# Kernel tuning notes

Measured on AMD Instinct MI355X. Metric: run time of the kernel, lower is better.

## Reference

```python
import jax, jax.numpy as jnp
import numpy as np

B, P, H, W, D, C = 16, 4, 32, 32, 32, 8


def setup_inputs() -> dict:
    key = jax.random.key(0)
    k1, k2 = jax.random.split(key)
    input_fmap = jax.random.normal(k1, (B, P, H, W, D, C), dtype=jnp.float32)
    # identity affine + small noise so sampled coords mostly stay in-volume
    ident = jnp.concatenate([jnp.eye(3, dtype=jnp.float32), jnp.zeros((3, 1), jnp.float32)], axis=1)
    theta = ident[None, None] + 0.05 * jax.random.normal(k2, (B, P, 3, 4), dtype=jnp.float32)
    return {"input_fmap": input_fmap, "theta": theta}


def _affine_grid(theta, H, W, D):
    # matches tf.meshgrid default 'xy' indexing: shapes (H, W, D)
    x = jnp.arange(W, dtype=jnp.float32)
    y = jnp.arange(H, dtype=jnp.float32)
    z = jnp.arange(D, dtype=jnp.float32)
    xt, yt, zt = jnp.meshgrid(x, y, z, indexing='xy')  # each (H, W, D)
    grid = jnp.stack([xt.ravel(), yt.ravel(), zt.ravel(), jnp.ones(H * W * D, jnp.float32)], axis=0)  # (4, HWD)
    bg = jnp.einsum('bpij,jn->bpin', theta, grid)  # (B, P, 3, HWD)
    return bg.reshape(theta.shape[0], theta.shape[1], 3, H, W, D)


def reference(input_fmap, theta):
    Bb, Pp, Hh, Ww, Dd, Cc = input_fmap.shape
    bg = _affine_grid(theta, Hh, Ww, Dd)
    x = bg[:, :, 0] + 2.0  # (B, P, H, W, D)
    y = bg[:, :, 1] + 2.0
    z = bg[:, :, 2] + 2.0
    padded = jnp.pad(input_fmap, ((0, 0), (0, 0), (2, 2), (2, 2), (2, 2), (0, 0)))
    # faithful to original: all three axes clipped with H+2 (cubic volume assumed)
    x0 = jnp.clip(jnp.floor(x).astype(jnp.int32), 0, Hh + 2)
    y0 = jnp.clip(jnp.floor(y).astype(jnp.int32), 0, Hh + 2)
    z0 = jnp.clip(jnp.floor(z).astype(jnp.int32), 0, Hh + 2)
    x1, y1, z1 = x0 + 1, y0 + 1, z0 + 1

    bi = jnp.arange(Bb)[:, None, None, None, None]
    pi = jnp.arange(Pp)[None, :, None, None, None]

    def gather(xi, yi, zi):
        # (B, P, H, W, D, C), indices applied to spatial dims with batch_dims=2
        return padded[bi, pi, xi, yi, zi]

    c000 = gather(x0, y0, z0)
    c001 = gather(x0, y0, z1)
    c010 = gather(x0, y1, z0)
    c011 = gather(x0, y1, z1)
    c100 = gather(x1, y0, z0)
    c101 = gather(x1, y0, z1)
    c110 = gather(x1, y1, z0)
    c111 = gather(x1, y1, z1)

    xd = (x - x0.astype(jnp.float32))[..., None]  # (B, P, H, W, D, 1)
    yd = (y - y0.astype(jnp.float32))[..., None]
    zd = (z - z0.astype(jnp.float32))[..., None]

    out = (c000 * (1 - xd) * (1 - yd) * (1 - zd)
           + c100 * xd * (1 - yd) * (1 - zd)
           + c010 * (1 - xd) * yd * (1 - zd)
           + c001 * (1 - xd) * (1 - yd) * zd
           + c101 * xd * (1 - yd) * zd
           + c011 * (1 - xd) * yd * zd
           + c110 * xd * yd * (1 - zd)
           + c111 * xd * yd * zd)
    return out
```

## Files before the change

### kernel.cpp

```cpp
#include <hip/hip_runtime.h>
#include <cstddef>

#define BB 16
#define PP 4
#define HH 32
#define WW 32
#define DD 32
#define CC 8

typedef float fx4 __attribute__((ext_vector_type(4)));

__global__ __launch_bounds__(256) void resample_kernel(
    const float* __restrict__ fmap,
    const float* __restrict__ theta,
    float* __restrict__ out)
{
    const int bp   = blockIdx.x >> 8;
    const int tid  = threadIdx.x;
    const int vox  = ((blockIdx.x & 255) << 7) | (tid >> 1);
    const int half = tid & 1;
    const int d = vox & 31;
    const int w = (vox >> 5) & 31;
    const int h = vox >> 10;

    const float* th = theta + bp * 12;
    const float fw = (float)w, fh = (float)h, fd = (float)d;
    const float x = fmaf(th[0], fw, fmaf(th[1], fh, fmaf(th[2],  fd, th[3] ))) + 2.0f;
    const float y = fmaf(th[4], fw, fmaf(th[5], fh, fmaf(th[6],  fd, th[7] ))) + 2.0f;
    const float z = fmaf(th[8], fw, fmaf(th[9], fh, fmaf(th[10], fd, th[11]))) + 2.0f;

    const int x0 = min(max((int)floorf(x), 0), HH + 2);
    const int y0 = min(max((int)floorf(y), 0), HH + 2);
    const int z0 = min(max((int)floorf(z), 0), HH + 2);
    const float xd = x - (float)x0, yd = y - (float)y0, zd = z - (float)z0;

    const int ix[2] = { x0 - 2, x0 - 1 };
    const int iy[2] = { y0 - 2, y0 - 1 };
    const int iz[2] = { z0 - 2, z0 - 1 };
    const float wxv[2] = { (1.0f - xd) * (((unsigned)ix[0] < (unsigned)HH) ? 1.0f : 0.0f),
                           xd          * (((unsigned)ix[1] < (unsigned)HH) ? 1.0f : 0.0f) };
    const float wyv[2] = { (1.0f - yd) * (((unsigned)iy[0] < (unsigned)WW) ? 1.0f : 0.0f),
                           yd          * (((unsigned)iy[1] < (unsigned)WW) ? 1.0f : 0.0f) };
    const float wzv[2] = { (1.0f - zd) * (((unsigned)iz[0] < (unsigned)DD) ? 1.0f : 0.0f),
                           zd          * (((unsigned)iz[1] < (unsigned)DD) ? 1.0f : 0.0f) };
    const int cx[2] = { min(max(ix[0], 0), HH - 1), min(max(ix[1], 0), HH - 1) };
    const int cy[2] = { min(max(iy[0], 0), WW - 1), min(max(iy[1], 0), WW - 1) };
    const int cz[2] = { min(max(iz[0], 0), DD - 1), min(max(iz[1], 0), DD - 1) };

    const float* __restrict__ base = fmap + (size_t)bp * (HH * WW * DD * CC) + half * 4;

    fx4   c[8];
    float wgt[8];
    #pragma unroll
    for (int i = 0; i < 8; ++i) {
        const int bx = (i >> 2) & 1, by = (i >> 1) & 1, bz = i & 1;
        const size_t off = (size_t)(((cx[bx] * WW + cy[by]) * DD + cz[bz]) * CC);
        c[i]   = *(const fx4*)(base + off);
        wgt[i] = wxv[bx] * wyv[by] * wzv[bz];
    }

    fx4 acc = (fx4){0.f, 0.f, 0.f, 0.f};
    #pragma unroll
    for (int i = 0; i < 8; ++i) {
        acc.x = fmaf(wgt[i], c[i].x, acc.x);
        acc.y = fmaf(wgt[i], c[i].y, acc.y);
        acc.z = fmaf(wgt[i], c[i].z, acc.z);
        acc.w = fmaf(wgt[i], c[i].w, acc.w);
    }

    fx4* o = (fx4*)(out + (size_t)(bp * (HH * WW * DD) + vox) * CC + half * 4);
    __builtin_nontemporal_store(acc, o);
}

extern "C" void kernel_launch(void* const* d_in, const int* in_sizes, int n_in,
                              void* d_out, int out_size, void* d_ws, size_t ws_size,
                              hipStream_t stream) {
    const float* fmap  = (const float*)d_in[0];
    const float* theta = (const float*)d_in[1];
    float* out = (float*)d_out;

    const int total_blocks = BB * PP * 256;
    resample_kernel<<<dim3(total_blocks), dim3(256), 0, stream>>>(fmap, theta, out);
}
```

Measured before the change: 122.4 us.

## Loop each thread over 16 h-slices with double-buffered gather prefetch

Each thread now processes 16 consecutive h positions instead of one voxel, and the grid shrinks accordingly. The loads for slice t+1 are issued before slice t is consumed, with schedule barriers to keep the overlap, and affine terms that do not depend on h are hoisted out of the loop. The aim is to hide gather latency and cut per-thread setup overhead. The cost is fewer resident waves, more registers per thread, and less parallelism across the grid.

After: 129.4 us. 1.06x slower.

```diff
diff --git a/kernel.cpp b/kernel.cpp
--- a/kernel.cpp
+++ b/kernel.cpp
@@ -7,6 +7,7 @@
 #define WW 32
 #define DD 32
 #define CC 8
+#define TT 16
 
 typedef float fx4 __attribute__((ext_vector_type(4)));
 
@@ -15,61 +16,92 @@
     const float* __restrict__ theta,
     float* __restrict__ out)
 {
-    const int bp   = blockIdx.x >> 8;
+    const int bp  = blockIdx.x >> 4;
+    const int hb  = (blockIdx.x >> 3) & 1;
+    const int wb  = blockIdx.x & 7;
     const int tid  = threadIdx.x;
-    const int vox  = ((blockIdx.x & 255) << 7) | (tid >> 1);
     const int half = tid & 1;
-    const int d = vox & 31;
-    const int w = (vox >> 5) & 31;
-    const int h = vox >> 10;
+    const int d    = (tid >> 1) & 31;
+    const int w    = (wb << 2) + (tid >> 6);
+    const int hbase = hb << 4;
 
     const float* th = theta + bp * 12;
-    const float fw = (float)w, fh = (float)h, fd = (float)d;
-    const float x = fmaf(th[0], fw, fmaf(th[1], fh, fmaf(th[2],  fd, th[3] ))) + 2.0f;
-    const float y = fmaf(th[4], fw, fmaf(th[5], fh, fmaf(th[6],  fd, th[7] ))) + 2.0f;
-    const float z = fmaf(th[8], fw, fmaf(th[9], fh, fmaf(th[10], fd, th[11]))) + 2.0f;
-
-    const int x0 = min(max((int)floorf(x), 0), HH + 2);
-    const int y0 = min(max((int)floorf(y), 0), HH + 2);
-    const int z0 = min(max((int)floorf(z), 0), HH + 2);
-    const float xd = x - (float)x0, yd = y - (float)y0, zd = z - (float)z0;
-
-    const int ix[2] = { x0 - 2, x0 - 1 };
-    const int iy[2] = { y0 - 2, y0 - 1 };
-    const int iz[2] = { z0 - 2, z0 - 1 };
-    const float wxv[2] = { (1.0f - xd) * (((unsigned)ix[0] < (unsigned)HH) ? 1.0f : 0.0f),
-                           xd          * (((unsigned)ix[1] < (unsigned)HH) ? 1.0f : 0.0f) };
-    const float wyv[2] = { (1.0f - yd) * (((unsigned)iy[0] < (unsigned)WW) ? 1.0f : 0.0f),
-                           yd          * (((unsigned)iy[1] < (unsigned)WW) ? 1.0f : 0.0f) };
-    const float wzv[2] = { (1.0f - zd) * (((unsigned)iz[0] < (unsigned)DD) ? 1.0f : 0.0f),
-                           zd          * (((unsigned)iz[1] < (unsigned)DD) ? 1.0f : 0.0f) };
-    const int cx[2] = { min(max(ix[0], 0), HH - 1), min(max(ix[1], 0), HH - 1) };
-    const int cy[2] = { min(max(iy[0], 0), WW - 1), min(max(iy[1], 0), WW - 1) };
-    const int cz[2] = { min(max(iz[0], 0), DD - 1), min(max(iz[1], 0), DD - 1) };
+    const float t1 = th[1], t5 = th[5], t9 = th[9];
+    const float fw = (float)w, fd = (float)d;
+    const float xw = fmaf(th[0], fw, fmaf(th[2],  fd, th[3] )) + 2.0f;
+    const float yw = fmaf(th[4], fw, fmaf(th[6],  fd, th[7] )) + 2.0f;
+    const float zw = fmaf(th[8], fw, fmaf(th[10], fd, th[11])) + 2.0f;
 
     const float* __restrict__ base = fmap + (size_t)bp * (HH * WW * DD * CC) + half * 4;
+    float* __restrict__ obase = out + (size_t)bp * (HH * WW * DD * CC)
+                                + (size_t)((hbase * WW + w) * DD + d) * CC + half * 4;
 
-    fx4   c[8];
-    float wgt[8];
+    auto calc = [&](int t, unsigned off[8], float wgt[8]) {
+        const float fh = (float)(hbase + t);
+        const float x = fmaf(t1, fh, xw);
+        const float y = fmaf(t5, fh, yw);
+        const float z = fmaf(t9, fh, zw);
+        const int x0 = min(max((int)floorf(x), 0), HH + 2);
+        const int y0 = min(max((int)floorf(y), 0), HH + 2);
+        const int z0 = min(max((int)floorf(z), 0), HH + 2);
+        const float xd = x - (float)x0, yd = y - (float)y0, zd = z - (float)z0;
+        const int ix[2] = { x0 - 2, x0 - 1 };
+        const int iy[2] = { y0 - 2, y0 - 1 };
+        const int iz[2] = { z0 - 2, z0 - 1 };
+        const float wxv[2] = { (1.0f - xd) * (((unsigned)ix[0] < (unsigned)HH) ? 1.0f : 0.0f),
+                               xd          * (((unsigned)ix[1] < (unsigned)HH) ? 1.0f : 0.0f) };
+        const float wyv[2] = { (1.0f - yd) * (((unsigned)iy[0] < (unsigned)WW) ? 1.0f : 0.0f),
+                               yd          * (((unsigned)iy[1] < (unsigned)WW) ? 1.0f : 0.0f) };
+        const float wzv[2] = { (1.0f - zd) * (((unsigned)iz[0] < (unsigned)DD) ? 1.0f : 0.0f),
+                               zd          * (((unsigned)iz[1] < (unsigned)DD) ? 1.0f : 0.0f) };
+        const unsigned ox[2] = { (unsigned)(min(max(ix[0], 0), HH - 1) * (WW * DD * CC)),
+                                 (unsigned)(min(max(ix[1], 0), HH - 1) * (WW * DD * CC)) };
+        const unsigned oy[2] = { (unsigned)(min(max(iy[0], 0), WW - 1) * (DD * CC)),
+                                 (unsigned)(min(max(iy[1], 0), WW - 1) * (DD * CC)) };
+        const unsigned oz[2] = { (unsigned)(min(max(iz[0], 0), DD - 1) * CC),
+                                 (unsigned)(min(max(iz[1], 0), DD - 1) * CC) };
+        #pragma unroll
+        for (int i = 0; i < 8; ++i) {
+            const int bx = (i >> 2) & 1, by = (i >> 1) & 1, bz = i & 1;
+            off[i] = ox[bx] + oy[by] + oz[bz];
+            wgt[i] = wxv[bx] * wyv[by] * wzv[bz];
+        }
+    };
+    auto loadv = [&](const unsigned off[8], fx4 c[8]) {
+        #pragma unroll
+        for (int i = 0; i < 8; ++i)
+            c[i] = *(const fx4*)(base + off[i]);
+    };
+    auto consume = [&](int t, const fx4 c[8], const float wgt[8]) {
+        fx4 acc = (fx4){0.f, 0.f, 0.f, 0.f};
+        #pragma unroll
+        for (int i = 0; i < 8; ++i) {
+            acc.x = fmaf(wgt[i], c[i].x, acc.x);
+            acc.y = fmaf(wgt[i], c[i].y, acc.y);
+            acc.z = fmaf(wgt[i], c[i].z, acc.z);
+            acc.w = fmaf(wgt[i], c[i].w, acc.w);
+        }
+        __builtin_nontemporal_store(acc, (fx4*)(obase + t * (WW * DD * CC)));
+    };
+
+    unsigned offA[8], offB[8];
+    float    wgtA[8], wgtB[8];
+    fx4      cA[8],   cB[8];
+
+    calc(0, offA, wgtA);
+    loadv(offA, cA);
+
     #pragma unroll
-    for (int i = 0; i < 8; ++i) {
-        const int bx = (i >> 2) & 1, by = (i >> 1) & 1, bz = i & 1;
-        const size_t off = (size_t)(((cx[bx] * WW + cy[by]) * DD + cz[bz]) * CC);
-        c[i]   = *(const fx4*)(base + off);
-        wgt[i] = wxv[bx] * wyv[by] * wzv[bz];
+    for (int t = 0; t < TT; ++t) {
+        const bool even = (t & 1) == 0;
+        if (t + 1 < TT) {
+            calc(t + 1, even ? offB : offA, even ? wgtB : wgtA);
+            loadv(even ? offB : offA, even ? cB : cA);
+        }
+        __builtin_amdgcn_sched_barrier(0);
+        consume(t, even ? cA : cB, even ? wgtA : wgtB);
+        __builtin_amdgcn_sched_barrier(0);
     }
-
-    fx4 acc = (fx4){0.f, 0.f, 0.f, 0.f};
-    #pragma unroll
-    for (int i = 0; i < 8; ++i) {
-        acc.x = fmaf(wgt[i], c[i].x, acc.x);
-        acc.y = fmaf(wgt[i], c[i].y, acc.y);
-        acc.z = fmaf(wgt[i], c[i].z, acc.z);
-        acc.w = fmaf(wgt[i], c[i].w, acc.w);
-    }
-
-    fx4* o = (fx4*)(out + (size_t)(bp * (HH * WW * DD) + vox) * CC + half * 4);
-    __builtin_nontemporal_store(acc, o);
 }
 
 extern "C" void kernel_launch(void* const* d_in, const int* in_sizes, int n_in,
@@ -79,6 +111,6 @@
     const float* theta = (const float*)d_in[1];
     float* out = (float*)d_out;
 
-    const int total_blocks = BB * PP * 256;
+    const int total_blocks = BB * PP * 16;
     resample_kernel<<<dim3(total_blocks), dim3(256), 0, stream>>>(fmap, theta, out);
 }
```
